# Kernel tuning notes

Measured on AMD Instinct MI355X. Metric: run time of the kernel, lower is better.

## Reference

```python
import jax, jax.numpy as jnp
import numpy as np

B, NUM_ROIS, NUM_GT = 32, 8192, 128
NUM_SAMPLED = 512
POS_FRAC = 0.25
BACKGROUND = 0.0
VARIANCE = np.array([0.1, 0.1, 0.2, 0.2], np.float32)  # [dy, dx, dh, dw]
IMG = 1024.0


def _make_boxes(key, shape):
    # valid yxyx boxes: positive height/width, inside image
    kc, ks = jax.random.split(key)
    c = jax.random.uniform(kc, shape[:-1] + (2,), minval=0.2, maxval=0.8) * IMG
    hw = jax.random.uniform(ks, shape[:-1] + (2,), minval=0.05, maxval=0.3) * IMG
    return jnp.concatenate([c - 0.5 * hw, c + 0.5 * hw], axis=-1)


def setup_inputs() -> dict:
    key = jax.random.key(0)
    k1, k2, k3, k4 = jax.random.split(key, 4)
    rois = _make_boxes(k1, (B, NUM_ROIS, 4))
    gt_boxes = _make_boxes(k2, (B, NUM_GT, 4))
    gt_classes = jax.random.randint(k3, (B, NUM_GT, 1), 1, 81).astype(jnp.float32)
    # uniform noise used by balanced_sample (channel 0 for positives, 1 for negatives)
    sample_noise = jax.random.uniform(k4, (B, NUM_ROIS + NUM_GT, 2), dtype=jnp.float32)
    return {"rois": rois, "gt_boxes": gt_boxes, "gt_classes": gt_classes,
            "sample_noise": sample_noise}


def _compute_iou(a, b):
    # a: [B,N,4], b: [B,G,4] in yxyx; use_masking=True -> padded (-1) boxes get iou=-1
    a_ = a[:, :, None, :]   # [B,N,1,4]
    b_ = b[:, None, :, :]   # [B,1,G,4]
    iy = jnp.maximum(jnp.minimum(a_[..., 2], b_[..., 2]) - jnp.maximum(a_[..., 0], b_[..., 0]), 0.0)
    ix = jnp.maximum(jnp.minimum(a_[..., 3], b_[..., 3]) - jnp.maximum(a_[..., 1], b_[..., 1]), 0.0)
    inter = iy * ix
    area_a = (a[..., 2] - a[..., 0]) * (a[..., 3] - a[..., 1])  # [B,N]
    area_b = (b[..., 2] - b[..., 0]) * (b[..., 3] - b[..., 1])  # [B,G]
    union = area_a[:, :, None] + area_b[:, None, :] - inter
    iou = inter / jnp.maximum(union, 1e-8)
    mask_a = jnp.all(a == -1.0, axis=-1)  # [B,N] padded rois
    mask_b = jnp.all(b == -1.0, axis=-1)  # [B,G] padded gt
    masked = mask_a[:, :, None] | mask_b[:, None, :]
    return jnp.where(masked, -1.0, iou)


def _encode_deltas(anchors, boxes):
    # yxyx -> (dy,dx,dh,dw)/variance
    ah = anchors[..., 2] - anchors[..., 0]
    aw = anchors[..., 3] - anchors[..., 1]
    acy = anchors[..., 0] + 0.5 * ah
    acx = anchors[..., 1] + 0.5 * aw
    bh = boxes[..., 2] - boxes[..., 0]
    bw = boxes[..., 3] - boxes[..., 1]
    bcy = boxes[..., 0] + 0.5 * bh
    bcx = boxes[..., 1] + 0.5 * bw
    d = jnp.stack([(bcy - acy) / ah, (bcx - acx) / aw,
                   jnp.log(bh / ah), jnp.log(bw / aw)], axis=-1)
    return d / jnp.asarray(VARIANCE, d.dtype)


def _balanced_sample(pos, neg, noise, num_samples, pos_frac):
    # returns float indicator [B,N]: 1.0 for sampled rois
    num_pos = int(num_samples * pos_frac)
    num_neg = num_samples - num_pos
    b, n = pos.shape
    pos_scores = jnp.where(pos, noise[..., 0], -1.0)
    neg_scores = jnp.where(neg, noise[..., 1], -1.0)
    _, pi = jax.lax.top_k(pos_scores, num_pos)
    _, ni = jax.lax.top_k(neg_scores, num_neg)
    rows = jnp.arange(b)[:, None]
    # only mark picks that are actually positive/negative (handles scarcity)
    pv = jnp.take_along_axis(pos, pi, axis=-1).astype(jnp.float32)
    nv = jnp.take_along_axis(neg, ni, axis=-1).astype(jnp.float32)
    ind = jnp.zeros((b, n), jnp.float32)
    ind = ind.at[rows, pi].add(pv)
    ind = ind.at[rows, ni].add(nv)  # pos/neg disjoint -> stays in {0,1}
    return ind


def _gather(t, idx):
    # t: [B,M,D], idx: [B,K] -> [B,K,D]
    return jnp.take_along_axis(t, idx[..., None], axis=1)


def reference(rois, gt_boxes, gt_classes, sample_noise):
    # append_gt_boxes=True
    rois_all = jnp.concatenate([rois, gt_boxes], axis=1)  # [B, N+G, 4]
    sim = _compute_iou(rois_all, gt_boxes)                # [B, N+G, G]
    matched_cols = jnp.argmax(sim, axis=-1)               # [B, N+G]
    max_iou = jnp.max(sim, axis=-1)
    # ArgmaxBoxMatcher(thresholds=[0.0,0.5], match_values=[-2,-1,1])
    matched_vals = jnp.where(max_iou >= 0.5, 1, jnp.where(max_iou >= 0.0, -1, -2))
    positive = matched_vals == 1
    negative = matched_vals == -1
    background = ~positive                                # [B, N+G]

    matched_gt_classes = _gather(gt_classes, matched_cols)
    matched_gt_classes = jnp.where(background[..., None], BACKGROUND, matched_gt_classes)
    matched_gt_boxes = _gather(gt_boxes, matched_cols)
    encoded = _encode_deltas(rois_all, matched_gt_boxes)
    encoded = jnp.where(background[..., None], 0.0, encoded)

    indicators = _balanced_sample(positive, negative, sample_noise, NUM_SAMPLED, POS_FRAC)
    sampled_indicators, sampled_idx = jax.lax.top_k(indicators, NUM_SAMPLED)

    sampled_rois = _gather(rois_all, sampled_idx)
    sampled_gt_boxes = _gather(encoded, sampled_idx)
    sampled_gt_classes = _gather(matched_gt_classes, sampled_idx)
    sampled_box_weights = _gather(positive[..., None].astype(gt_boxes.dtype), sampled_idx)
    sampled_class_weights = sampled_indicators[..., None].astype(gt_classes.dtype)
    return (sampled_rois, sampled_gt_boxes, sampled_box_weights,
            sampled_gt_classes, sampled_class_weights)
```

## Files before the change

kernel.cpp:

```cpp
#include <hip/hip_runtime.h>
#include <cstdint>

#define NB 32
#define NROIS 8192
#define NGT 128
#define NALL (NROIS + NGT)
#define NSAMP 512
#define KPOS 128
#define KNEG 384
#define BCAP 1024
#define TS 1024
#define CH 9

__global__ __launch_bounds__(128) void k_match(
    const float* __restrict__ rois,
    const float* __restrict__ gt,
    const float* __restrict__ noise,
    int* __restrict__ mword)
{
  __shared__ float4 sg[NGT];
  __shared__ float sab[NGT];
  __shared__ unsigned long long smask[2];

  const int b = blockIdx.y;
  const int tid = threadIdx.x;
  const float4* gt4 = reinterpret_cast<const float4*>(gt) + (size_t)b * NGT;

  float4 g0 = gt4[tid];
  sg[tid] = g0;
  sab[tid] = (g0.z - g0.x) * (g0.w - g0.y);
  const bool mflag = (g0.x == -1.0f) && (g0.y == -1.0f) && (g0.z == -1.0f) && (g0.w == -1.0f);
  const unsigned long long mb = __ballot(mflag);
  if ((tid & 63) == 0) smask[tid >> 6] = mb;
  __syncthreads();
  const bool anymask = (smask[0] | smask[1]) != 0ULL;

  const int i = blockIdx.x * 128 + tid;
  float4 A = (blockIdx.x < 64)
    ? (reinterpret_cast<const float4*>(rois) + (size_t)b * NROIS)[i]
    : sg[tid];
  const float aar = (A.z - A.x) * (A.w - A.y);
  const bool ma = (A.x == -1.0f) && (A.y == -1.0f) && (A.z == -1.0f) && (A.w == -1.0f);

  int cc;
  int code;

  if (!anymask && __ballot(ma) == 0ULL) {
    float bi[4], bu[4];
    int bc[4];
    #pragma unroll
    for (int c = 0; c < 4; ++c) { bi[c] = 0.0f; bu[c] = 1.0f; bc[c] = c * 32; }

    #pragma unroll 8
    for (int jj = 0; jj < 32; ++jj) {
      #pragma unroll
      for (int c = 0; c < 4; ++c) {
        const int j = c * 32 + jj;
        const float4 g = sg[j];
        const float ab = sab[j];
        float iy = fmaxf(fminf(A.z, g.z) - fmaxf(A.x, g.x), 0.0f);
        float ix = fmaxf(fminf(A.w, g.w) - fmaxf(A.y, g.y), 0.0f);
        float inter = iy * ix;
        float uc = fmaxf((aar + ab) - inter, 1e-8f);
        const bool win = (inter * bu[c]) > (bi[c] * uc);
        bi[c] = win ? inter : bi[c];
        bu[c] = win ? uc : bu[c];
        bc[c] = win ? j : bc[c];
      }
    }
    float qi = bi[0], qu = bu[0];
    cc = bc[0];
    #pragma unroll
    for (int c = 1; c < 4; ++c) {
      const bool win = (bi[c] * qu) > (qi * bu[c]);
      qi = win ? bi[c] : qi;
      qu = win ? bu[c] : qu;
      cc = win ? bc[c] : cc;
    }
    {
      #pragma clang fp contract(off)
      const float4 g = sg[cc];
      float iy = fmaxf(fminf(A.z, g.z) - fmaxf(A.x, g.x), 0.0f);
      float ix = fmaxf(fminf(A.w, g.w) - fmaxf(A.y, g.y), 0.0f);
      float inter = iy * ix;
      float ab = (g.z - g.x) * (g.w - g.y);
      float uni = (aar + ab) - inter;
      float bb = inter / fmaxf(uni, 1e-8f);
      code = (bb >= 0.5f) ? 3 : ((bb >= 0.0f) ? 1 : 0);
    }
  } else {
    #pragma clang fp contract(off)
    float bb = -3.0e38f; cc = 0;
    for (int j = 0; j < NGT; ++j) {
      float4 gg = sg[j];
      const bool mj = (gg.x == -1.0f) && (gg.y == -1.0f) && (gg.z == -1.0f) && (gg.w == -1.0f);
      float iy = fmaxf(fminf(A.z, gg.z) - fmaxf(A.x, gg.x), 0.0f);
      float ix = fmaxf(fminf(A.w, gg.w) - fmaxf(A.y, gg.y), 0.0f);
      float inter = iy * ix;
      float uni = (aar + sab[j]) - inter;
      float iou = inter / fmaxf(uni, 1e-8f);
      if (ma || mj) iou = -1.0f;
      if (iou > bb) { bb = iou; cc = j; }
    }
    code = (bb >= 0.5f) ? 3 : ((bb >= 0.0f) ? 1 : 0);
  }

  float2 nz = reinterpret_cast<const float2*>(noise)[(size_t)b * NALL + i];
  float v = (code == 3) ? nz.x : nz.y;
  int bin = (int)(v * 1024.0f);
  bin = bin < 0 ? 0 : (bin > 1023 ? 1023 : bin);
  mword[(size_t)b * NALL + i] = cc | (code << 7) | (bin << 9);
}

__device__ __forceinline__ int block_incl_scan(int v, int tid, int* wsum) {
  __syncthreads();
  int s = v;
  #pragma unroll
  for (int off = 1; off < 64; off <<= 1) {
    int u = __shfl_up(s, off);
    if ((tid & 63) >= off) s += u;
  }
  const int wid = tid >> 6;
  if ((tid & 63) == 63) wsum[wid] = s;
  __syncthreads();
  if (wid == 0) {
    const int lane = tid & 63;
    int w = (lane < (TS >> 6)) ? wsum[lane] : 0;
    #pragma unroll
    for (int off = 1; off < (TS >> 6); off <<= 1) {
      int u = __shfl_up(w, off);
      if (lane >= off) w += u;
    }
    if (lane < (TS >> 6)) wsum[lane] = w;
  }
  __syncthreads();
  return s + (wid ? wsum[wid - 1] : 0);
}

__global__ __launch_bounds__(TS) void k_select(
    const int* __restrict__ mword,
    const float* __restrict__ noise,
    const float* __restrict__ rois,
    const float* __restrict__ gt,
    const float* __restrict__ gtcls,
    float* __restrict__ out)
{
  #pragma clang fp contract(off)
  const int b = blockIdx.x;
  const int tid = threadIdx.x;

  __shared__ int hist[1024];
  __shared__ int wsum[TS >> 6];
  __shared__ int s_total;
  __shared__ float bval[2][BCAP];
  __shared__ int bidx_[2][BCAP];
  __shared__ int bcnt[2];
  __shared__ int s_bstar[2], s_need[2];
  __shared__ unsigned char ind[NALL];
  __shared__ unsigned short sorder[NSAMP];

  int ew[CH];

  hist[tid] = 0;
  if (tid < 2) bcnt[tid] = 0;

  #pragma unroll
  for (int k = 0; k < CH; ++k) {
    const int i = tid + k * TS;
    int w = 0;
    if (i < NALL) {
      ind[i] = 0;
      w = mword[(size_t)b * NALL + i];
    }
    ew[k] = w;
  }
  __syncthreads();
  #pragma unroll
  for (int k = 0; k < CH; ++k) {
    const int w = ew[k];
    if (w & 0x80) atomicAdd(&hist[w >> 9], (w & 0x100) ? 1 : (1 << 16));
  }
  __syncthreads();

  const int c = hist[tid];
  const int incl = block_incl_scan(c, tid, wsum);
  if (tid == TS - 1) s_total = incl;
  __syncthreads();
  const int total = s_total;

  #pragma unroll
  for (int p = 0; p < 2; ++p) {
    const int want = p ? KNEG : KPOS;
    const int sh = p ? 16 : 0;
    const int tot = (total >> sh) & 0xFFFF;
    if (tot >= want) {
      const int inc = (incl >> sh) & 0xFFFF;
      const int cp = (c >> sh) & 0xFFFF;
      const int above = tot - inc;
      if (above < want && above + cp >= want) {
        s_bstar[p] = tid; s_need[p] = want - above;
      }
    }
  }
  __syncthreads();

  const bool selall0 = ((total & 0xFFFF) < KPOS);
  const bool selall1 = (((total >> 16) & 0xFFFF) < KNEG);

  #pragma unroll
  for (int k = 0; k < CH; ++k) {
    const int w = ew[k];
    if (w & 0x80) {
      const int i = tid + k * TS;
      const int p = (w & 0x100) ? 0 : 1;
      const bool selall = p ? selall1 : selall0;
      const int bin = w >> 9;
      if (selall || bin > s_bstar[p]) {
        ind[i] = 1;
      } else if (bin == s_bstar[p]) {
        int pos = atomicAdd(&bcnt[p], 1);
        if (pos < BCAP) {
          bval[p][pos] = noise[((size_t)b * NALL + i) * 2 + p];
          bidx_[p][pos] = i;
        }
      }
    }
  }
  __syncthreads();

  #pragma unroll
  for (int p = 0; p < 2; ++p) {
    const bool selall = p ? selall1 : selall0;
    if (selall) continue;
    int cnt = bcnt[p]; if (cnt > BCAP) cnt = BCAP;
    const int need = s_need[p];
    for (int x = tid; x < cnt; x += TS) {
      const float v = bval[p][x];
      const int id = bidx_[p][x];
      int rank = 0;
      for (int y = 0; y < cnt; ++y) {
        const float vy = bval[p][y];
        const int iy2 = bidx_[p][y];
        rank += (vy > v) || (vy == v && iy2 < id);
      }
      if (rank < need) ind[id] = 1;
    }
  }
  __syncthreads();

  const int start = tid * CH;
  const int end = (start + CH < NALL) ? (start + CH) : NALL;
  int cnt1 = 0;
  for (int i = start; i < end; ++i) cnt1 += ind[i];
  const int incl1 = block_incl_scan(cnt1, tid, wsum);
  if (tid == TS - 1) s_total = incl1;
  __syncthreads();
  const int K1 = s_total;
  int ones_before = incl1 - cnt1;
  const int nzero = NSAMP - K1;
  for (int i = start; i < end; ++i) {
    if (ind[i]) {
      sorder[ones_before] = (unsigned short)i;
      ones_before++;
    } else {
      const int zrank = i - ones_before;
      if (zrank < nzero) sorder[K1 + zrank] = (unsigned short)i;
    }
  }
  __syncthreads();

  if (tid < NSAMP) {
    const int s = tid;
    const int idx = sorder[s];
    const size_t t = (size_t)b * NSAMP + s;

    float4 A = (idx < NROIS)
      ? reinterpret_cast<const float4*>(rois)[(size_t)b * NROIS + idx]
      : reinterpret_cast<const float4*>(gt)[(size_t)b * NGT + (idx - NROIS)];

    const int w = mword[(size_t)b * NALL + idx];
    const int col = w & 0x7F;
    const bool pos = (((w >> 7) & 3) == 3);

    float e0 = 0.f, e1 = 0.f, e2 = 0.f, e3 = 0.f, cls = 0.f;
    if (pos) {
      float4 G = reinterpret_cast<const float4*>(gt)[(size_t)b * NGT + col];
      float ah = A.z - A.x, aw = A.w - A.y;
      float acy = A.x + 0.5f * ah, acx = A.y + 0.5f * aw;
      float bh = G.z - G.x, bw = G.w - G.y;
      float bcy = G.x + 0.5f * bh, bcx = G.y + 0.5f * bw;
      e0 = ((bcy - acy) / ah) / 0.1f;
      e1 = ((bcx - acx) / aw) / 0.1f;
      e2 = logf(bh / ah) / 0.2f;
      e3 = logf(bw / aw) / 0.2f;
      cls = gtcls[(size_t)b * NGT + col];
    }

    float* o_rois = out;
    float* o_enc  = out + (size_t)NB * NSAMP * 4;
    float* o_bw   = out + (size_t)NB * NSAMP * 8;
    float* o_cls  = o_bw + (size_t)NB * NSAMP;
    float* o_cw   = o_cls + (size_t)NB * NSAMP;

    reinterpret_cast<float4*>(o_rois)[t] = A;
    float4 E; E.x = e0; E.y = e1; E.z = e2; E.w = e3;
    reinterpret_cast<float4*>(o_enc)[t] = E;
    o_bw[t]  = pos ? 1.0f : 0.0f;
    o_cls[t] = cls;
    o_cw[t]  = (s < K1) ? 1.0f : 0.0f;
  }
}

extern "C" void kernel_launch(void* const* d_in, const int* in_sizes, int n_in,
                              void* d_out, int out_size, void* d_ws, size_t ws_size,
                              hipStream_t stream) {
  const float* rois  = (const float*)d_in[0];
  const float* gt    = (const float*)d_in[1];
  const float* gtcls = (const float*)d_in[2];
  const float* noise = (const float*)d_in[3];
  float* out = (float*)d_out;

  int* mword = (int*)d_ws;

  dim3 g1(NALL / 128, NB);
  k_match<<<g1, 128, 0, stream>>>(rois, gt, noise, mword);
  k_select<<<NB, TS, 0, stream>>>(mword, noise, rois, gt, gtcls, out);
}
```

Before: 38.93 us.

## Split matching into a cheap positive-candidate filter and an exact argmax pass

The first matching kernel now only checks whether any ground-truth box could give IoU >= 0.5. It uses the division-free bound 3*inter - area_b >= area_a, with a safety margin. Rois that cannot match are written straight out as negatives with their noise bin. Candidates are appended with atomics to a per-batch list, and a second kernel runs the full argmax IoU only on that list. This removes the argmax bookkeeping for most rois, at the cost of an extra memset, an extra kernel launch and atomic contention on the per-batch counters.

```diff
diff --git a/kernel.cpp b/kernel.cpp
--- a/kernel.cpp
+++ b/kernel.cpp
@@ -16,7 +16,9 @@
     const float* __restrict__ rois,
     const float* __restrict__ gt,
     const float* __restrict__ noise,
-    int* __restrict__ mword)
+    int* __restrict__ mword,
+    int* __restrict__ flcnt,
+    int* __restrict__ fllist)
 {
   __shared__ float4 sg[NGT];
   __shared__ float sab[NGT];
@@ -25,6 +27,7 @@
   const int b = blockIdx.y;
   const int tid = threadIdx.x;
   const float4* gt4 = reinterpret_cast<const float4*>(gt) + (size_t)b * NGT;
+  const float4* rois4 = reinterpret_cast<const float4*>(rois) + (size_t)b * NROIS;
 
   float4 g0 = gt4[tid];
   sg[tid] = g0;
@@ -36,61 +39,49 @@
   const bool anymask = (smask[0] | smask[1]) != 0ULL;
 
   const int i = blockIdx.x * 128 + tid;
-  float4 A = (blockIdx.x < 64)
-    ? (reinterpret_cast<const float4*>(rois) + (size_t)b * NROIS)[i]
-    : sg[tid];
+  float4 A = (blockIdx.x < 64) ? rois4[i] : sg[tid];
   const float aar = (A.z - A.x) * (A.w - A.y);
   const bool ma = (A.x == -1.0f) && (A.y == -1.0f) && (A.z == -1.0f) && (A.w == -1.0f);
 
-  int cc;
-  int code;
-
   if (!anymask && __ballot(ma) == 0ULL) {
-    float bi[4], bu[4];
-    int bc[4];
-    #pragma unroll
-    for (int c = 0; c < 4; ++c) { bi[c] = 0.0f; bu[c] = 1.0f; bc[c] = c * 32; }
-
-    #pragma unroll 8
-    for (int jj = 0; jj < 32; ++jj) {
+    float m0 = -3.0e38f, m1 = -3.0e38f;
+    for (int jo = 0; jo < 64; jo += 32) {
+      const float4* p0 = &sg[jo];
+      const float4* p1 = &sg[jo + 64];
+      const float* a0 = &sab[jo];
+      const float* a1 = &sab[jo + 64];
       #pragma unroll
-      for (int c = 0; c < 4; ++c) {
-        const int j = c * 32 + jj;
-        const float4 g = sg[j];
-        const float ab = sab[j];
-        float iy = fmaxf(fminf(A.z, g.z) - fmaxf(A.x, g.x), 0.0f);
-        float ix = fmaxf(fminf(A.w, g.w) - fmaxf(A.y, g.y), 0.0f);
-        float inter = iy * ix;
-        float uc = fmaxf((aar + ab) - inter, 1e-8f);
-        const bool win = (inter * bu[c]) > (bi[c] * uc);
-        bi[c] = win ? inter : bi[c];
-        bu[c] = win ? uc : bu[c];
-        bc[c] = win ? j : bc[c];
+      for (int jj = 0; jj < 32; ++jj) {
+        {
+          const float4 g = p0[jj];
+          float iy = fmaxf(fminf(A.z, g.z) - fmaxf(A.x, g.x), 0.0f);
+          float ix = fmaxf(fminf(A.w, g.w) - fmaxf(A.y, g.y), 0.0f);
+          float inter = iy * ix;
+          m0 = fmaxf(m0, fmaf(3.0f, inter, -a0[jj]));
+        }
+        {
+          const float4 g = p1[jj];
+          float iy = fmaxf(fminf(A.z, g.z) - fmaxf(A.x, g.x), 0.0f);
+          float ix = fmaxf(fminf(A.w, g.w) - fmaxf(A.y, g.y), 0.0f);
+          float inter = iy * ix;
+          m1 = fmaxf(m1, fmaf(3.0f, inter, -a1[jj]));
+        }
       }
     }
-    float qi = bi[0], qu = bu[0];
-    cc = bc[0];
-    #pragma unroll
-    for (int c = 1; c < 4; ++c) {
-      const bool win = (bi[c] * qu) > (qi * bu[c]);
-      qi = win ? bi[c] : qi;
-      qu = win ? bu[c] : qu;
-      cc = win ? bc[c] : cc;
-    }
-    {
-      #pragma clang fp contract(off)
-      const float4 g = sg[cc];
-      float iy = fmaxf(fminf(A.z, g.z) - fmaxf(A.x, g.x), 0.0f);
-      float ix = fmaxf(fminf(A.w, g.w) - fmaxf(A.y, g.y), 0.0f);
-      float inter = iy * ix;
-      float ab = (g.z - g.x) * (g.w - g.y);
-      float uni = (aar + ab) - inter;
-      float bb = inter / fmaxf(uni, 1e-8f);
-      code = (bb >= 0.5f) ? 3 : ((bb >= 0.0f) ? 1 : 0);
+    const bool flagged = fmaxf(m0, m1) >= (aar - 16.0f);
+    if (flagged) {
+      const int p = atomicAdd(&flcnt[b], 1);
+      fllist[(size_t)b * NALL + p] = i;
+    } else {
+      float2 nz = reinterpret_cast<const float2*>(noise)[(size_t)b * NALL + i];
+      int bin = (int)(nz.y * 1024.0f);
+      bin = bin < 0 ? 0 : (bin > 1023 ? 1023 : bin);
+      mword[(size_t)b * NALL + i] = (1 << 7) | (bin << 9);
     }
   } else {
     #pragma clang fp contract(off)
-    float bb = -3.0e38f; cc = 0;
+    float bb = -3.0e38f;
+    int cc = 0;
     for (int j = 0; j < NGT; ++j) {
       float4 gg = sg[j];
       const bool mj = (gg.x == -1.0f) && (gg.y == -1.0f) && (gg.z == -1.0f) && (gg.w == -1.0f);
@@ -102,9 +93,81 @@
       if (ma || mj) iou = -1.0f;
       if (iou > bb) { bb = iou; cc = j; }
     }
+    int code = (bb >= 0.5f) ? 3 : ((bb >= 0.0f) ? 1 : 0);
+    float2 nz = reinterpret_cast<const float2*>(noise)[(size_t)b * NALL + i];
+    float v = (code == 3) ? nz.x : nz.y;
+    int bin = (int)(v * 1024.0f);
+    bin = bin < 0 ? 0 : (bin > 1023 ? 1023 : bin);
+    mword[(size_t)b * NALL + i] = cc | (code << 7) | (bin << 9);
+  }
+}
+
+__global__ __launch_bounds__(256) void k_match2(
+    const float* __restrict__ rois,
+    const float* __restrict__ gt,
+    const float* __restrict__ noise,
+    const int* __restrict__ flcnt,
+    const int* __restrict__ fllist,
+    int* __restrict__ mword)
+{
+  const int b = blockIdx.y;
+  const int cnt = flcnt[b];
+  const int base = blockIdx.x * 256 + threadIdx.x;
+  if (blockIdx.x * 256 >= cnt) return;
+
+  __shared__ float4 sg[NGT];
+  const float4* gt4 = reinterpret_cast<const float4*>(gt) + (size_t)b * NGT;
+  if (threadIdx.x < NGT) sg[threadIdx.x] = gt4[threadIdx.x];
+  __syncthreads();
+
+  if (base >= cnt) return;
+  const int i = fllist[(size_t)b * NALL + base];
+  const float4* rois4 = reinterpret_cast<const float4*>(rois) + (size_t)b * NROIS;
+  float4 A = (i < NROIS) ? rois4[i] : sg[i - NROIS];
+  const float aar = (A.z - A.x) * (A.w - A.y);
+
+  float bi[4], bu[4];
+  int bc[4];
+  #pragma unroll
+  for (int c = 0; c < 4; ++c) { bi[c] = 0.0f; bu[c] = 1.0f; bc[c] = c * 32; }
+
+  #pragma unroll 8
+  for (int jj = 0; jj < 32; ++jj) {
+    #pragma unroll
+    for (int c = 0; c < 4; ++c) {
+      const int j = c * 32 + jj;
+      const float4 g = sg[j];
+      const float ab = (g.z - g.x) * (g.w - g.y);
+      float iy = fmaxf(fminf(A.z, g.z) - fmaxf(A.x, g.x), 0.0f);
+      float ix = fmaxf(fminf(A.w, g.w) - fmaxf(A.y, g.y), 0.0f);
+      float inter = iy * ix;
+      float uc = fmaxf((aar + ab) - inter, 1e-8f);
+      const bool win = (inter * bu[c]) > (bi[c] * uc);
+      bi[c] = win ? inter : bi[c];
+      bu[c] = win ? uc : bu[c];
+      bc[c] = win ? j : bc[c];
+    }
+  }
+  float qi = bi[0], qu = bu[0];
+  int cc = bc[0];
+  #pragma unroll
+  for (int c = 1; c < 4; ++c) {
+    const bool win = (bi[c] * qu) > (qi * bu[c]);
+    qi = win ? bi[c] : qi; qu = win ? bu[c] : qu; cc = win ? bc[c] : cc;
+  }
+
+  int code;
+  {
+    #pragma clang fp contract(off)
+    const float4 g = sg[cc];
+    float iy = fmaxf(fminf(A.z, g.z) - fmaxf(A.x, g.x), 0.0f);
+    float ix = fmaxf(fminf(A.w, g.w) - fmaxf(A.y, g.y), 0.0f);
+    float inter = iy * ix;
+    float ab = (g.z - g.x) * (g.w - g.y);
+    float uni = (aar + ab) - inter;
+    float bb = inter / fmaxf(uni, 1e-8f);
     code = (bb >= 0.5f) ? 3 : ((bb >= 0.0f) ? 1 : 0);
   }
-
   float2 nz = reinterpret_cast<const float2*>(noise)[(size_t)b * NALL + i];
   float v = (code == 3) ? nz.x : nz.y;
   int bin = (int)(v * 1024.0f);
@@ -320,9 +383,16 @@
   const float* noise = (const float*)d_in[3];
   float* out = (float*)d_out;
 
-  int* mword = (int*)d_ws;
+  uint8_t* ws = (uint8_t*)d_ws;
+  int* mword  = (int*)ws;
+  int* fllist = mword + (size_t)NB * NALL;
+  int* flcnt  = fllist + (size_t)NB * NALL;
+
+  hipMemsetAsync(flcnt, 0, NB * sizeof(int), stream);
 
   dim3 g1(NALL / 128, NB);
-  k_match<<<g1, 128, 0, stream>>>(rois, gt, noise, mword);
+  k_match<<<g1, 128, 0, stream>>>(rois, gt, noise, mword, flcnt, fllist);
+  dim3 g2((NALL + 255) / 256, NB);
+  k_match2<<<g2, 256, 0, stream>>>(rois, gt, noise, flcnt, fllist, mword);
   k_select<<<NB, TS, 0, stream>>>(mword, noise, rois, gt, gtcls, out);
 }
```

After: 92.04 us. 2.36x slower.
